# Optimization experiments

Measured on AMD Instinct MI355X. Metric: run time of the kernel, lower is better.

Reference implementation:

```python
import jax, jax.numpy as jnp
import numpy as np

N = 2048  # number of graph nodes


def setup_inputs() -> dict:
    key = jax.random.key(0)
    k1, k2, k3, k4 = jax.random.split(key, 4)
    # dense non-negative adjacency / association matrix
    A = jax.random.uniform(k1, (N, N), dtype=jnp.float32)
    # GTConv weights: layer0.conv1, layer0.conv2, layer1.conv1 (each (2,1,1,1))
    w1a = jax.random.normal(k2, (2, 1, 1, 1), dtype=jnp.float32)
    w1b = jax.random.normal(k3, (2, 1, 1, 1), dtype=jnp.float32)
    w2a = jax.random.normal(k4, (2, 1, 1, 1), dtype=jnp.float32)
    return {"A": A, "w1a": w1a, "w1b": w1b, "w2a": w2a}


def _gtconv(A4, w):
    # A4: (1,1,n,n); w: (2,1,1,1). softmax over dim=1 (singleton -> ones),
    # broadcast-multiply -> (2,1,n,n), sum over dim 0 -> (1,n,n)
    sw = jax.nn.softmax(w, axis=1)
    return jnp.sum(A4 * sw, axis=0)


def _norm(H):
    # H: (n,n). H <- diag(deg)^-1 @ (H + I), expressed as a row-scale
    # (identical math to the diagonal mm in the original).
    n = H.shape[0]
    H = H + jnp.eye(n, dtype=H.dtype)
    deg = jnp.sum(H, axis=1)
    deg = jnp.where(deg <= 1e-10, jnp.ones_like(deg), deg)
    return H / deg[:, None]


def reference(A, w1a, w1b, w2a):
    A4 = A[None, None]  # (1,1,n,n) after the forward's unsqueeze + broadcast
    # layer 0 (first=True)
    a = _gtconv(A4, w1a)            # (1,n,n)
    b = _gtconv(A4, w1b)            # (1,n,n)
    H = jnp.matmul(a, b)            # (1,n,n)
    # layer 1 (first=False): normalization of H[0], then bmm with conv(A)
    H_ = _norm(H[0])[None]          # (1,n,n)
    a2 = _gtconv(A4, w2a)           # (1,n,n)
    H2 = jnp.matmul(H_, a2)         # (1,n,n)
    return H2
```

## Files before the change

kernel.cpp:

```cpp
#include <hip/hip_runtime.h>
#include <stdint.h>

#define N 2048
#define TM 128
#define TN 64
#define BK 32
#define KI (N / BK)
#define LDSW 40
#define ABUF 5120
#define BBUF 2560
#define BOFF (2 * ABUF)
#define NN ((size_t)N * (size_t)N)

typedef unsigned short u16;
typedef __bf16 bf16x8 __attribute__((ext_vector_type(8)));
typedef unsigned short ushortx8 __attribute__((ext_vector_type(8)));
typedef float floatx4 __attribute__((ext_vector_type(4)));

static __device__ __forceinline__ u16 f2bf(float f) {
  unsigned int u = __builtin_bit_cast(unsigned int, f);
  return (u16)((u + 0x7fffu + ((u >> 16) & 1u)) >> 16);
}

__global__ void cast_tr(const float* __restrict__ A, u16* __restrict__ Ab,
                        u16* __restrict__ Abt) {
  __shared__ float tile[32][33];
  const int tx = threadIdx.x, ty = threadIdx.y;
  const int c = blockIdx.x * 32 + tx;
#pragma unroll
  for (int i = 0; i < 4; i++) {
    const int r = blockIdx.y * 32 + ty + i * 8;
    const float v = A[r * N + c];
    Ab[r * N + c] = f2bf(v);
    tile[ty + i * 8][tx] = v;
  }
  __syncthreads();
  const int r2 = blockIdx.y * 32 + tx;
#pragma unroll
  for (int i = 0; i < 4; i++) {
    const int c2 = blockIdx.x * 32 + ty + i * 8;
    Abt[c2 * N + r2] = f2bf(tile[tx][ty + i * 8]);
  }
}

__device__ __forceinline__ void gemm_core(u16* smem, const u16* __restrict__ L,
                                          const u16* __restrict__ Rt,
                                          floatx4 acc[4][2]) {
  const int t = threadIdx.x;
  const int row0 = blockIdx.y * TM;
  const int col0 = blockIdx.x * TN;

  const int srA = t >> 1;
  const int scA = (t & 1) * 16;
  const u16* gA = L + (size_t)(row0 + srA) * N + scA;
  const int wbA = srA * LDSW + scA;
  const int srB = t >> 2;
  const int scB = (t & 3) * 8;
  const u16* gB = Rt + (size_t)(col0 + srB) * N + scB;
  const int wbB = BOFF + srB * LDSW + scB;

  const int lane = t & 63;
  const int w = t >> 6;
  const int wr = (w >> 1) * 64;
  const int wc = (w & 1) * 32;
  const int lr = lane & 15;
  const int q = lane >> 4;
  const int raA = (wr + lr) * LDSW + q * 8;
  const int raB = BOFF + (wc + lr) * LDSW + q * 8;

#pragma unroll
  for (int i = 0; i < 4; i++)
#pragma unroll
    for (int j = 0; j < 2; j++) acc[i][j] = (floatx4){0.f, 0.f, 0.f, 0.f};

  ushortx8 rA[4][2], rB[4];
#pragma unroll
  for (int s = 0; s < 3; s++) {
    rA[s][0] = *(const ushortx8*)(gA + s * BK);
    rA[s][1] = *(const ushortx8*)(gA + s * BK + 8);
    rB[s] = *(const ushortx8*)(gB + s * BK);
  }
  *(ushortx8*)(&smem[wbA]) = rA[0][0];
  *(ushortx8*)(&smem[wbA + 8]) = rA[0][1];
  *(ushortx8*)(&smem[wbB]) = rB[0];
  __syncthreads();

#define GSTEP(i, s)                                                           \
  {                                                                           \
    if ((i) + 3 < KI) {                                                       \
      rA[((s) + 3) & 3][0] = *(const ushortx8*)(gA + ((i) + 3) * BK);         \
      rA[((s) + 3) & 3][1] = *(const ushortx8*)(gA + ((i) + 3) * BK + 8);     \
      rB[((s) + 3) & 3] = *(const ushortx8*)(gB + ((i) + 3) * BK);            \
    }                                                                         \
    bf16x8 af[4], bq[2];                                                      \
    _Pragma("unroll") for (int mt = 0; mt < 4; mt++) af[mt] =                 \
        __builtin_bit_cast(bf16x8, *(const ushortx8*)&smem[                   \
            raA + ((s) & 1) * ABUF + mt * 16 * LDSW]);                        \
    _Pragma("unroll") for (int nt = 0; nt < 2; nt++) bq[nt] =                 \
        __builtin_bit_cast(bf16x8, *(const ushortx8*)&smem[                   \
            raB + ((s) & 1) * BBUF + nt * 16 * LDSW]);                        \
    _Pragma("unroll") for (int mt = 0; mt < 4; mt++)                          \
        _Pragma("unroll") for (int nt = 0; nt < 2; nt++) acc[mt][nt] =        \
            __builtin_amdgcn_mfma_f32_16x16x32_bf16(af[mt], bq[nt],           \
                                                    acc[mt][nt], 0, 0, 0);    \
    __syncthreads();   \
    if ((i) + 1 < KI) {                                                       \
      *(ushortx8*)(&smem[wbA + (((s) + 1) & 1) * ABUF]) = rA[((s) + 1) & 3][0]; \
      *(ushortx8*)(&smem[wbA + (((s) + 1) & 1) * ABUF + 8]) =                 \
          rA[((s) + 1) & 3][1];                                               \
      *(ushortx8*)(&smem[wbB + (((s) + 1) & 1) * BBUF]) = rB[((s) + 1) & 3];  \
    }                                                                         \
    __syncthreads();                   \
  }

  for (int io = 0; io < KI; io += 4) {
    GSTEP(io + 0, 0)
    GSTEP(io + 1, 1)
    GSTEP(io + 2, 2)
    GSTEP(io + 3, 3)
  }
#undef GSTEP
}

__global__ __launch_bounds__(256, 2) void gemm1(const u16* __restrict__ Ab,
                                                const u16* __restrict__ Abt,
                                                u16* __restrict__ Mb,
                                                float* __restrict__ deg) {
  __shared__ __align__(16) u16 smem[2 * ABUF + 2 * BBUF];
  floatx4 acc[4][2];
  gemm_core(smem, Ab, Abt, acc);

  float* rs = (float*)smem;
  const int t = threadIdx.x;
  const int row0 = blockIdx.y * TM, col0 = blockIdx.x * TN;
  if (t < TM) rs[t] = 0.f;
  __syncthreads();
  const int lane = t & 63, w = t >> 6;
  const int wr = (w >> 1) * 64, wc = (w & 1) * 32;
  const int lr = lane & 15, q = lane >> 4;
  float trs[4][4];
#pragma unroll
  for (int mt = 0; mt < 4; mt++)
#pragma unroll
    for (int r = 0; r < 4; r++) trs[mt][r] = 0.f;
#pragma unroll
  for (int mt = 0; mt < 4; mt++)
#pragma unroll
    for (int nt = 0; nt < 2; nt++)
#pragma unroll
      for (int r = 0; r < 4; r++) {
        const float v = acc[mt][nt][r];
        const int rr = row0 + wr + mt * 16 + q * 4 + r;
        const int cc = col0 + wc + nt * 16 + lr;
        Mb[(size_t)rr * N + cc] = f2bf(v);
        trs[mt][r] += v;
      }
#pragma unroll
  for (int mt = 0; mt < 4; mt++)
#pragma unroll
    for (int r = 0; r < 4; r++)
      atomicAdd(&rs[wr + mt * 16 + q * 4 + r], trs[mt][r]);
  __syncthreads();
  if (t < TM) atomicAdd(&deg[row0 + t], rs[t]);
}

__global__ __launch_bounds__(256, 2) void gemm2(const u16* __restrict__ Mb,
                                                const u16* __restrict__ Abt,
                                                const float* __restrict__ A,
                                                const float* __restrict__ deg,
                                                float* __restrict__ out) {
  __shared__ __align__(16) u16 smem[2 * ABUF + 2 * BBUF];
  floatx4 acc[4][2];
  gemm_core(smem, Mb, Abt, acc);

  const int t = threadIdx.x;
  const int row0 = blockIdx.y * TM, col0 = blockIdx.x * TN;
  const int lane = t & 63, w = t >> 6;
  const int wr = (w >> 1) * 64, wc = (w & 1) * 32;
  const int lr = lane & 15, q = lane >> 4;
#pragma unroll
  for (int mt = 0; mt < 4; mt++)
#pragma unroll
    for (int r = 0; r < 4; r++) {
      const int rr = row0 + wr + mt * 16 + q * 4 + r;
      float d = 4.f * deg[rr] + 1.f;
      if (d <= 1e-10f) d = 1.f;
      const float rd = 1.f / d;
#pragma unroll
      for (int nt = 0; nt < 2; nt++) {
        const int cc = col0 + wc + nt * 16 + lr;
        out[(size_t)rr * N + cc] =
            (8.f * acc[mt][nt][r] + 2.f * A[(size_t)rr * N + cc]) * rd;
      }
    }
}

extern "C" void kernel_launch(void* const* d_in, const int* in_sizes, int n_in,
                              void* d_out, int out_size, void* d_ws, size_t ws_size,
                              hipStream_t stream) {
  const float* A = (const float*)d_in[0];
  float* out = (float*)d_out;
  char* ws = (char*)d_ws;
  u16* Ab = (u16*)ws;
  u16* Abt = (u16*)(ws + NN * 2);
  u16* Mb = (u16*)(ws + NN * 4);
  float* deg = (float*)(ws + NN * 6);

  hipMemsetAsync(deg, 0, N * sizeof(float), stream);
  cast_tr<<<dim3(N / 32, N / 32), dim3(32, 8), 0, stream>>>(A, Ab, Abt);
  gemm1<<<dim3(N / TN, N / TM), 256, 0, stream>>>(Ab, Abt, Mb, deg);
  gemm2<<<dim3(N / TN, N / TM), 256, 0, stream>>>(Mb, Abt, A, deg, out);
}
```

Measured before the change: 158.2 us.

## Use 128x128 tiles with 512 threads, single barrier per k-step, vectorized cast

```diff
diff --git a/kernel.cpp b/kernel.cpp
--- a/kernel.cpp
+++ b/kernel.cpp
@@ -2,19 +2,18 @@
 #include <stdint.h>
 
 #define N 2048
-#define TM 128
-#define TN 64
+#define TILE 128
 #define BK 32
 #define KI (N / BK)
 #define LDSW 40
-#define ABUF 5120
-#define BBUF 2560
+#define ABUF (TILE * LDSW)
 #define BOFF (2 * ABUF)
 #define NN ((size_t)N * (size_t)N)
 
 typedef unsigned short u16;
 typedef __bf16 bf16x8 __attribute__((ext_vector_type(8)));
 typedef unsigned short ushortx8 __attribute__((ext_vector_type(8)));
+typedef unsigned short ushortx4 __attribute__((ext_vector_type(4)));
 typedef float floatx4 __attribute__((ext_vector_type(4)));
 
 static __device__ __forceinline__ u16 f2bf(float f) {
@@ -25,44 +24,43 @@
 __global__ void cast_tr(const float* __restrict__ A, u16* __restrict__ Ab,
                         u16* __restrict__ Abt) {
   __shared__ float tile[32][33];
-  const int tx = threadIdx.x, ty = threadIdx.y;
-  const int c = blockIdx.x * 32 + tx;
-#pragma unroll
-  for (int i = 0; i < 4; i++) {
-    const int r = blockIdx.y * 32 + ty + i * 8;
-    const float v = A[r * N + c];
-    Ab[r * N + c] = f2bf(v);
-    tile[ty + i * 8][tx] = v;
-  }
+  const int u = threadIdx.x;
+  const int r = u >> 3;
+  const int c4 = (u & 7) * 4;
+  const int gr = blockIdx.y * 32 + r;
+  const int gc = blockIdx.x * 32 + c4;
+  const float4 v = *(const float4*)(A + (size_t)gr * N + gc);
+  ushortx4 o;
+  o[0] = f2bf(v.x); o[1] = f2bf(v.y); o[2] = f2bf(v.z); o[3] = f2bf(v.w);
+  *(ushortx4*)(Ab + (size_t)gr * N + gc) = o;
+  tile[r][c4 + 0] = v.x; tile[r][c4 + 1] = v.y;
+  tile[r][c4 + 2] = v.z; tile[r][c4 + 3] = v.w;
   __syncthreads();
-  const int r2 = blockIdx.y * 32 + tx;
-#pragma unroll
-  for (int i = 0; i < 4; i++) {
-    const int c2 = blockIdx.x * 32 + ty + i * 8;
-    Abt[c2 * N + r2] = f2bf(tile[tx][ty + i * 8]);
-  }
+  const int tc = u >> 3;
+  const int rc = (u & 7) * 4;
+  ushortx4 w;
+#pragma unroll
+  for (int j = 0; j < 4; j++) w[j] = f2bf(tile[rc + j][tc]);
+  *(ushortx4*)(Abt + (size_t)(blockIdx.x * 32 + tc) * N + blockIdx.y * 32 + rc) = w;
 }
 
 __device__ __forceinline__ void gemm_core(u16* smem, const u16* __restrict__ L,
                                           const u16* __restrict__ Rt,
                                           floatx4 acc[4][2]) {
   const int t = threadIdx.x;
-  const int row0 = blockIdx.y * TM;
-  const int col0 = blockIdx.x * TN;
-
-  const int srA = t >> 1;
-  const int scA = (t & 1) * 16;
-  const u16* gA = L + (size_t)(row0 + srA) * N + scA;
-  const int wbA = srA * LDSW + scA;
-  const int srB = t >> 2;
-  const int scB = (t & 3) * 8;
-  const u16* gB = Rt + (size_t)(col0 + srB) * N + scB;
-  const int wbB = BOFF + srB * LDSW + scB;
+  const int row0 = blockIdx.y * TILE;
+  const int col0 = blockIdx.x * TILE;
+
+  const int srow = t >> 2;
+  const int sc = (t & 3) * 8;
+  const u16* gA = L + (size_t)(row0 + srow) * N + sc;
+  const u16* gB = Rt + (size_t)(col0 + srow) * N + sc;
+  const int wb = srow * LDSW + sc;
 
   const int lane = t & 63;
   const int w = t >> 6;
-  const int wr = (w >> 1) * 64;
-  const int wc = (w & 1) * 32;
+  const int wr = (w >> 2) * 64;
+  const int wc = (w & 3) * 32;
   const int lr = lane & 15;
   const int q = lane >> 4;
   const int raA = (wr + lr) * LDSW + q * 8;
@@ -73,44 +71,38 @@
 #pragma unroll
     for (int j = 0; j < 2; j++) acc[i][j] = (floatx4){0.f, 0.f, 0.f, 0.f};
 
-  ushortx8 rA[4][2], rB[4];
+  ushortx8 rA[4], rB[4];
 #pragma unroll
   for (int s = 0; s < 3; s++) {
-    rA[s][0] = *(const ushortx8*)(gA + s * BK);
-    rA[s][1] = *(const ushortx8*)(gA + s * BK + 8);
+    rA[s] = *(const ushortx8*)(gA + s * BK);
     rB[s] = *(const ushortx8*)(gB + s * BK);
   }
-  *(ushortx8*)(&smem[wbA]) = rA[0][0];
-  *(ushortx8*)(&smem[wbA + 8]) = rA[0][1];
-  *(ushortx8*)(&smem[wbB]) = rB[0];
-  __syncthreads();
+  *(ushortx8*)(&smem[wb]) = rA[0];
+  *(ushortx8*)(&smem[BOFF + wb]) = rB[0];
 
 #define GSTEP(i, s)                                                           \
   {                                                                           \
     if ((i) + 3 < KI) {                                                       \
-      rA[((s) + 3) & 3][0] = *(const ushortx8*)(gA + ((i) + 3) * BK);         \
-      rA[((s) + 3) & 3][1] = *(const ushortx8*)(gA + ((i) + 3) * BK + 8);     \
+      rA[((s) + 3) & 3] = *(const ushortx8*)(gA + ((i) + 3) * BK);            \
       rB[((s) + 3) & 3] = *(const ushortx8*)(gB + ((i) + 3) * BK);            \
     }                                                                         \
+    __syncthreads();                     \
     bf16x8 af[4], bq[2];                                                      \
     _Pragma("unroll") for (int mt = 0; mt < 4; mt++) af[mt] =                 \
         __builtin_bit_cast(bf16x8, *(const ushortx8*)&smem[                   \
             raA + ((s) & 1) * ABUF + mt * 16 * LDSW]);                        \
     _Pragma("unroll") for (int nt = 0; nt < 2; nt++) bq[nt] =                 \
         __builtin_bit_cast(bf16x8, *(const ushortx8*)&smem[                   \
-            raB + ((s) & 1) * BBUF + nt * 16 * LDSW]);                        \
+            raB + ((s) & 1) * ABUF + nt * 16 * LDSW]);                        \
     _Pragma("unroll") for (int mt = 0; mt < 4; mt++)                          \
         _Pragma("unroll") for (int nt = 0; nt < 2; nt++) acc[mt][nt] =        \
             __builtin_amdgcn_mfma_f32_16x16x32_bf16(af[mt], bq[nt],           \
                                                     acc[mt][nt], 0, 0, 0);    \
-    __syncthreads();   \
     if ((i) + 1 < KI) {                                                       \
-      *(ushortx8*)(&smem[wbA + (((s) + 1) & 1) * ABUF]) = rA[((s) + 1) & 3][0]; \
-      *(ushortx8*)(&smem[wbA + (((s) + 1) & 1) * ABUF + 8]) =                 \
-          rA[((s) + 1) & 3][1];                                               \
-      *(ushortx8*)(&smem[wbB + (((s) + 1) & 1) * BBUF]) = rB[((s) + 1) & 3];  \
+      const int nb = (((s) + 1) & 1) * ABUF;                                  \
+      *(ushortx8*)(&smem[wb + nb]) = rA[((s) + 1) & 3];                       \
+      *(ushortx8*)(&smem[BOFF + wb + nb]) = rB[((s) + 1) & 3];                \
     }                                                                         \
-    __syncthreads();                   \
   }
 
   for (int io = 0; io < KI; io += 4) {
@@ -122,21 +114,21 @@
 #undef GSTEP
 }
 
-__global__ __launch_bounds__(256, 2) void gemm1(const u16* __restrict__ Ab,
+__global__ __launch_bounds__(512, 2) void gemm1(const u16* __restrict__ Ab,
                                                 const u16* __restrict__ Abt,
                                                 u16* __restrict__ Mb,
                                                 float* __restrict__ deg) {
-  __shared__ __align__(16) u16 smem[2 * ABUF + 2 * BBUF];
+  __shared__ __align__(16) u16 smem[4 * ABUF];
   floatx4 acc[4][2];
   gemm_core(smem, Ab, Abt, acc);
 
   float* rs = (float*)smem;
   const int t = threadIdx.x;
-  const int row0 = blockIdx.y * TM, col0 = blockIdx.x * TN;
-  if (t < TM) rs[t] = 0.f;
+  const int row0 = blockIdx.y * TILE, col0 = blockIdx.x * TILE;
+  if (t < TILE) rs[t] = 0.f;
   __syncthreads();
   const int lane = t & 63, w = t >> 6;
-  const int wr = (w >> 1) * 64, wc = (w & 1) * 32;
+  const int wr = (w >> 2) * 64, wc = (w & 3) * 32;
   const int lr = lane & 15, q = lane >> 4;
   float trs[4][4];
 #pragma unroll
@@ -161,22 +153,22 @@
     for (int r = 0; r < 4; r++)
       atomicAdd(&rs[wr + mt * 16 + q * 4 + r], trs[mt][r]);
   __syncthreads();
-  if (t < TM) atomicAdd(&deg[row0 + t], rs[t]);
-}
-
-__global__ __launch_bounds__(256, 2) void gemm2(const u16* __restrict__ Mb,
+  if (t < TILE) atomicAdd(&deg[row0 + t], rs[t]);
+}
+
+__global__ __launch_bounds__(512, 2) void gemm2(const u16* __restrict__ Mb,
                                                 const u16* __restrict__ Abt,
                                                 const float* __restrict__ A,
                                                 const float* __restrict__ deg,
                                                 float* __restrict__ out) {
-  __shared__ __align__(16) u16 smem[2 * ABUF + 2 * BBUF];
+  __shared__ __align__(16) u16 smem[4 * ABUF];
   floatx4 acc[4][2];
   gemm_core(smem, Mb, Abt, acc);
 
   const int t = threadIdx.x;
-  const int row0 = blockIdx.y * TM, col0 = blockIdx.x * TN;
+  const int row0 = blockIdx.y * TILE, col0 = blockIdx.x * TILE;
   const int lane = t & 63, w = t >> 6;
-  const int wr = (w >> 1) * 64, wc = (w & 1) * 32;
+  const int wr = (w >> 2) * 64, wc = (w & 3) * 32;
   const int lr = lane & 15, q = lane >> 4;
 #pragma unroll
   for (int mt = 0; mt < 4; mt++)
@@ -207,7 +199,7 @@
   float* deg = (float*)(ws + NN * 6);
 
   hipMemsetAsync(deg, 0, N * sizeof(float), stream);
-  cast_tr<<<dim3(N / 32, N / 32), dim3(32, 8), 0, stream>>>(A, Ab, Abt);
-  gemm1<<<dim3(N / TN, N / TM), 256, 0, stream>>>(Ab, Abt, Mb, deg);
-  gemm2<<<dim3(N / TN, N / TM), 256, 0, stream>>>(Mb, Abt, A, deg, out);
-}
+  cast_tr<<<dim3(N / 32, N / 32), 256, 0, stream>>>(A, Ab, Abt);
+  gemm1<<<dim3(N / TILE, N / TILE), 512, 0, stream>>>(Ab, Abt, Mb, deg);
+  gemm2<<<dim3(N / TILE, N / TILE), 512, 0, stream>>>(Mb, Abt, A, deg, out);
+}
```

After: 142.7 us. 9.8% less time.
